# Kernel tuning notes

Measured on AMD Instinct MI355X. Metric: run time of the kernel, lower is better.

## Reference

```python
import jax, jax.numpy as jnp
import numpy as np

DIM = 256
HEADS = 8
DIM_HEAD = 32
WS = 8  # window_size
INNER = HEADS * DIM_HEAD
SCALE = DIM_HEAD ** -0.5


def _rel_indices():
    # (WS^2, WS^2, 2) relative position indices, shifted to be non-negative
    idx = np.array([[x, y] for x in range(WS) for y in range(WS)])
    rel = idx[None, :, :] - idx[:, None, :] + (WS - 1)
    return jnp.asarray(rel, dtype=jnp.int32)


def setup_inputs() -> dict:
    key = jax.random.key(0)
    k1, k2, k3, k4 = jax.random.split(key, 4)
    x = jax.random.normal(k1, (2, 4, 128, 128, DIM), dtype=jnp.float32)
    w_qkv = jax.random.normal(k2, (DIM, 3 * INNER), dtype=jnp.float32) * 0.02
    pos_emb = jax.random.normal(k3, (2 * WS - 1, 2 * WS - 1), dtype=jnp.float32)
    w_out = jax.random.normal(k4, (INNER, DIM), dtype=jnp.float32) * 0.02
    b_out = jnp.zeros((DIM,), dtype=jnp.float32)
    return {"x": x, "w_qkv": w_qkv, "pos_emb": pos_emb, "w_out": w_out, "b_out": b_out}


def reference(x, w_qkv, pos_emb, w_out, b_out):
    B, L, H, W, C = x.shape
    nh, nw = H // WS, W // WS
    qkv = x @ w_qkv  # (B,L,H,W,3*INNER)
    q, k, v = jnp.split(qkv, 3, axis=-1)

    def to_windows(t):
        # (B,L,H,W,INNER) -> (B,L,m,nh*nw,WS*WS,DIM_HEAD)
        t = t.reshape(B, L, nh, WS, nw, WS, HEADS, DIM_HEAD)
        t = t.transpose(0, 1, 6, 2, 4, 3, 5, 7)
        return t.reshape(B, L, HEADS, nh * nw, WS * WS, DIM_HEAD)

    q, k, v = to_windows(q), to_windows(k), to_windows(v)

    rel = _rel_indices()
    bias = pos_emb[rel[..., 0], rel[..., 1]]  # (WS^2, WS^2)

    dots = jnp.einsum('blmhic,blmhjc->blmhij', q, k) * SCALE + bias
    attn = jax.nn.softmax(dots, axis=-1)
    out = jnp.einsum('blmhij,blmhjc->blmhic', attn, v)

    # inverse window rearrange: (B,L,m,nh*nw,WS*WS,c) -> (B,L,H,W,INNER)
    out = out.reshape(B, L, HEADS, nh, nw, WS, WS, DIM_HEAD)
    out = out.transpose(0, 1, 3, 5, 4, 6, 2, 7).reshape(B, L, H, W, INNER)
    return out @ w_out + b_out
```

## Files before the change

### kernel.cpp

```cpp
#include <hip/hip_runtime.h>
#include <hip/hip_bf16.h>


typedef __attribute__((ext_vector_type(8))) short bf16x8;
typedef __attribute__((ext_vector_type(4))) float f32x4;

__device__ __forceinline__ f32x4 mfma16(bf16x8 a, bf16x8 b, f32x4 c) {
  return __builtin_amdgcn_mfma_f32_16x16x32_bf16(a, b, c, 0, 0, 0);
}

__device__ __forceinline__ unsigned short f2bf(float f) {
  __hip_bfloat16 h = __float2bfloat16(f);
  return *reinterpret_cast<unsigned short*>(&h);
}

__device__ __forceinline__ uint2 pack4(float a, float b, float c, float d) {
  union { unsigned short u[4]; uint2 v; } pk;
  pk.u[0] = f2bf(a); pk.u[1] = f2bf(b); pk.u[2] = f2bf(c); pk.u[3] = f2bf(d);
  return pk.v;
}

#define LOG2E 1.4426950408889634f
#define EXPSCALE (0.17677669529663687f * 1.4426950408889634f)

#define XSTR 264
#define VSTR 72
#define SSTR 72
#define OFF_A  0
#define OFF_B  18432
#define OFF_SC 35328
#define SMEM_ELTS 39936

__global__ void prep_kernel(const float* __restrict__ w_qkv,
                            const float* __restrict__ w_out,
                            const float* __restrict__ pos_emb,
                            unsigned short* __restrict__ wqkvT,
                            unsigned short* __restrict__ woutT,
                            float* __restrict__ bias64) {
  const int stride = gridDim.x * blockDim.x;
  const int tid = blockIdx.x * blockDim.x + threadIdx.x;
  for (int i = tid; i < 768 * 256; i += stride) {
    int n = i >> 8, k = i & 255;
    int off = ((((n >> 4) * 8 + (k >> 5)) * 4 + ((k >> 3) & 3)) * 16 + (n & 15)) * 8 + (k & 7);
    wqkvT[off] = f2bf(w_qkv[k * 768 + n]);
  }
  for (int i = tid; i < 256 * 256; i += stride) {
    int n = i >> 8, k = i & 255;
    int off = ((((n >> 4) * 8 + (k >> 5)) * 4 + ((k >> 3) & 3)) * 16 + (n & 15)) * 8 + (k & 7);
    woutT[off] = f2bf(w_out[k * 256 + n]);
  }
  for (int i = tid; i < 64 * 64; i += stride) {
    int a = i >> 6, b = i & 63;
    int d0 = (b >> 3) - (a >> 3) + 7;
    int d1 = (b & 7) - (a & 7) + 7;
    bias64[i] = pos_emb[d0 * 15 + d1] * LOG2E;
  }
}

template <bool SWAP>
__device__ __forceinline__ void qkv_gemm(f32x4 (&acc)[4][4],
                                         const unsigned short* __restrict__ x_lds,
                                         const unsigned short* __restrict__ wqkvT,
                                         int col0, int l15, int lq) {
  const f32x4 zero4 = {0.f, 0.f, 0.f, 0.f};
#pragma unroll
  for (int rt = 0; rt < 4; ++rt)
#pragma unroll
    for (int ct = 0; ct < 4; ++ct) acc[rt][ct] = zero4;

  bf16x8 aP[4], bP[4], aN[4], bN[4];
#pragma unroll
  for (int rt = 0; rt < 4; ++rt)
    aP[rt] = *(const bf16x8*)&x_lds[(rt * 16 + l15) * XSTR + lq * 8];
#pragma unroll
  for (int ct = 0; ct < 4; ++ct)
    bP[ct] = *(const bf16x8*)&wqkvT[(((col0 >> 4) + ct) * 32 + lq) * 128 + l15 * 8];
#pragma unroll
  for (int kk = 0; kk < 8; ++kk) {
    if (kk < 7) {
      const int ko = (kk + 1) * 32 + lq * 8;
#pragma unroll
      for (int rt = 0; rt < 4; ++rt)
        aN[rt] = *(const bf16x8*)&x_lds[(rt * 16 + l15) * XSTR + ko];
#pragma unroll
      for (int ct = 0; ct < 4; ++ct)
        bN[ct] = *(const bf16x8*)&wqkvT[((((col0 >> 4) + ct) * 8 + kk + 1) * 4 + lq) * 128 + l15 * 8];
    }
#pragma unroll
    for (int rt = 0; rt < 4; ++rt)
#pragma unroll
      for (int ct = 0; ct < 4; ++ct)
        acc[rt][ct] = SWAP ? mfma16(bP[ct], aP[rt], acc[rt][ct])
                           : mfma16(aP[rt], bP[ct], acc[rt][ct]);
#pragma unroll
    for (int rt = 0; rt < 4; ++rt) aP[rt] = aN[rt];
#pragma unroll
    for (int ct = 0; ct < 4; ++ct) bP[ct] = bN[ct];
  }
}

__global__ __launch_bounds__(256, 2)
void winattn_kernel(const float* __restrict__ x,
                    const unsigned short* __restrict__ wqkvT,
                    const unsigned short* __restrict__ woutT,
                    const float* __restrict__ bias64,
                    const float* __restrict__ b_out,
                    float* __restrict__ out) {
  __shared__ unsigned short smem[SMEM_ELTS];

  const int tid = threadIdx.x;
  const int lane = tid & 63;
  const int w = tid >> 6;
  const int l15 = lane & 15;
  const int lq = lane >> 4;

  const int bid = blockIdx.x;
  const int win = bid & 255;
  const int img = bid >> 8;
  const int wy = win >> 4, wx = win & 15;

  unsigned short* x_lds  = smem + OFF_A;
  unsigned short* vT_lds = smem + OFF_A;
  unsigned short* qk_lds = smem + OFF_B;
  unsigned short* sc = smem + OFF_SC + w * (16 * SSTR);

  const f32x4 zero4 = {0.f, 0.f, 0.f, 0.f};
  const size_t img_base = (size_t)img * 128 * 128 * 256;

  {
#pragma unroll
    for (int r = 0; r < 16; ++r) {
      int p = r * 4 + w;
      const float* src = x + img_base +
          (((size_t)(wy * 8 + (p >> 3)) * 128) + (wx * 8 + (p & 7))) * 256 + lane * 4;
      float4 v4 = *(const float4*)src;
      *(uint2*)&x_lds[p * XSTR + lane * 4] = pack4(v4.x, v4.y, v4.z, v4.w);
    }
  }
  __syncthreads();

  {
    f32x4 acc[4][4];
    qkv_gemm<true>(acc, x_lds, wqkvT, w * 64, l15, lq);
#pragma unroll
    for (int rt = 0; rt < 4; ++rt)
#pragma unroll
      for (int ct = 0; ct < 4; ++ct)
        *(uint2*)&qk_lds[(rt * 16 + l15) * XSTR + w * 64 + ct * 16 + lq * 4] =
            pack4(acc[rt][ct][0], acc[rt][ct][1], acc[rt][ct][2], acc[rt][ct][3]);
  }
  __syncthreads();

  bf16x8 qf[8];
#pragma unroll
  for (int h = 0; h < 8; ++h)
    qf[h] = *(const bf16x8*)&qk_lds[(w * 16 + l15) * XSTR + h * 32 + lq * 8];

  {
    f32x4 kacc[4][4];
    qkv_gemm<true>(kacc, x_lds, wqkvT, 256 + w * 64, l15, lq);
    __syncthreads();
#pragma unroll
    for (int rt = 0; rt < 4; ++rt)
#pragma unroll
      for (int ct = 0; ct < 4; ++ct)
        *(uint2*)&qk_lds[(rt * 16 + l15) * XSTR + w * 64 + ct * 16 + lq * 4] =
            pack4(kacc[rt][ct][0], kacc[rt][ct][1], kacc[rt][ct][2], kacc[rt][ct][3]);
  }

  {
    f32x4 vacc[4][4];
    qkv_gemm<false>(vacc, x_lds, wqkvT, 512 + w * 64, l15, lq);
    __syncthreads();
#pragma unroll
    for (int rt = 0; rt < 4; ++rt)
#pragma unroll
      for (int ct = 0; ct < 4; ++ct)
        *(uint2*)&vT_lds[(w * 64 + ct * 16 + l15) * VSTR + rt * 16 + lq * 4] =
            pack4(vacc[rt][ct][0], vacc[rt][ct][1], vacc[rt][ct][2], vacc[rt][ct][3]);
  }
  __syncthreads();

  f32x4 bias4[4];
#pragma unroll
  for (int rt = 0; rt < 4; ++rt)
    bias4[rt] = *(const f32x4*)&bias64[(w * 16 + l15) * 64 + rt * 16 + lq * 4];

  const short one_bf = (short)0x3F80;
  const bf16x8 ones = {one_bf, one_bf, one_bf, one_bf,
                       one_bf, one_bf, one_bf, one_bf};

  f32x4 ACC[16];
#pragma unroll
  for (int ct = 0; ct < 16; ++ct) ACC[ct] = zero4;

  f32x4 s_t[4];
#pragma unroll
  for (int rt = 0; rt < 4; ++rt) {
    const bf16x8 bk = *(const bf16x8*)&qk_lds[(rt * 16 + l15) * XSTR + lq * 8];
    f32x4 t = mfma16(bk, qf[0], zero4);
#pragma unroll
    for (int r = 0; r < 4; ++r)
      s_t[rt][r] = __builtin_amdgcn_exp2f(t[r] * EXPSCALE + bias4[rt][r]);
  }

#pragma unroll
  for (int h = 0; h < 8; ++h) {
#pragma unroll
    for (int rt = 0; rt < 4; ++rt)
      *(uint2*)&sc[l15 * SSTR + rt * 16 + lq * 4] =
          pack4(s_t[rt][0], s_t[rt][1], s_t[rt][2], s_t[rt][3]);

    f32x4 sn[4];
    if (h < 7) {
#pragma unroll
      for (int rt = 0; rt < 4; ++rt) {
        const bf16x8 bk = *(const bf16x8*)&qk_lds[(rt * 16 + l15) * XSTR + (h + 1) * 32 + lq * 8];
        f32x4 t = mfma16(bk, qf[h + 1], zero4);
#pragma unroll
        for (int r = 0; r < 4; ++r)
          sn[rt][r] = __builtin_amdgcn_exp2f(t[r] * EXPSCALE + bias4[rt][r]);
      }
    }

    const bf16x8 ap0 = *(const bf16x8*)&sc[l15 * SSTR + lq * 8];
    const bf16x8 ap1 = *(const bf16x8*)&sc[l15 * SSTR + 32 + lq * 8];
    bf16x8 bw[16];
#pragma unroll
    for (int ct = 0; ct < 16; ++ct)
      bw[ct] = *(const bf16x8*)&woutT[((ct * 8 + h) * 4 + lq) * 128 + l15 * 8];

    f32x4 o0 = zero4, o1 = zero4, osum = zero4;
    {
      const bf16x8 bv00 = *(const bf16x8*)&vT_lds[(h * 32 + l15) * VSTR + lq * 8];
      const bf16x8 bv01 = *(const bf16x8*)&vT_lds[(h * 32 + l15) * VSTR + 32 + lq * 8];
      const bf16x8 bv10 = *(const bf16x8*)&vT_lds[(h * 32 + 16 + l15) * VSTR + lq * 8];
      const bf16x8 bv11 = *(const bf16x8*)&vT_lds[(h * 32 + 16 + l15) * VSTR + 32 + lq * 8];
      o0 = mfma16(bv00, ap0, o0);  o0 = mfma16(bv01, ap1, o0);
      o1 = mfma16(bv10, ap0, o1);  o1 = mfma16(bv11, ap1, o1);
      osum = mfma16(ones, ap0, osum);
      osum = mfma16(ones, ap1, osum);
    }

    const float rinv = __builtin_amdgcn_rcpf(osum[0]);
    *(uint2*)&sc[l15 * SSTR + lq * 4] =
        pack4(o0[0] * rinv, o0[1] * rinv, o0[2] * rinv, o0[3] * rinv);
    *(uint2*)&sc[l15 * SSTR + 16 + lq * 4] =
        pack4(o1[0] * rinv, o1[1] * rinv, o1[2] * rinv, o1[3] * rinv);

    const bf16x8 ao = *(const bf16x8*)&sc[l15 * SSTR + lq * 8];
#pragma unroll
    for (int ct = 0; ct < 16; ++ct)
      ACC[ct] = mfma16(bw[ct], ao, ACC[ct]);

    if (h < 7) {
#pragma unroll
      for (int rt = 0; rt < 4; ++rt) s_t[rt] = sn[rt];
    }
  }

  {
    const int p = w * 16 + l15;
    float* orow = out + img_base +
        (((size_t)(wy * 8 + (p >> 3)) * 128) + (wx * 8 + (p & 7))) * 256;
#pragma unroll
    for (int ct = 0; ct < 16; ++ct) {
      const int n0 = ct * 16 + lq * 4;
      const f32x4 bo4 = *(const f32x4*)&b_out[n0];
      f32x4 st;
#pragma unroll
      for (int r = 0; r < 4; ++r) st[r] = ACC[ct][r] + bo4[r];
      *(f32x4*)(orow + n0) = st;
    }
  }
}

extern "C" void kernel_launch(void* const* d_in, const int* in_sizes, int n_in,
                              void* d_out, int out_size, void* d_ws, size_t ws_size,
                              hipStream_t stream) {
  const float* x       = (const float*)d_in[0];
  const float* w_qkv   = (const float*)d_in[1];
  const float* pos_emb = (const float*)d_in[2];
  const float* w_out   = (const float*)d_in[3];
  const float* b_out   = (const float*)d_in[4];
  float* out = (float*)d_out;

  unsigned short* wqkvT = (unsigned short*)d_ws;
  unsigned short* woutT = wqkvT + 768 * 256;
  float* bias64 = (float*)(woutT + 256 * 256);

  prep_kernel<<<96, 256, 0, stream>>>(w_qkv, w_out, pos_emb, wqkvT, woutT, bias64);
  winattn_kernel<<<2048, 256, 0, stream>>>(x, wqkvT, woutT, bias64, b_out, out);
}
```

Before: 132.4 us.

## Restructure window attention so each wave owns two heads, keeping Q/K/V in registers

Each wave now computes Q, K and V for its own two heads in 32-column chunks and moves them into MFMA fragment registers through a small per-wave LDS transpose buffer. Shared LDS staging of Q/K/V is gone, cutting LDS use enough to raise launch bounds to three blocks per CU. Softmax row sums now use cross-lane shuffles instead of an extra ones-MFMA. The output projection becomes a separate block-wide GEMM over head outputs staged in LDS, so the per-head woutT reloads disappear. In exchange the kernel carries more register pressure, drops the explicit software prefetch in the GEMM, and adds a synchronization before the final projection.

Measured after the change: 116.6 us (median of 2 runs). 1.14x faster.

```diff
diff --git a/kernel.cpp b/kernel.cpp
--- a/kernel.cpp
+++ b/kernel.cpp
@@ -23,13 +23,12 @@
 #define LOG2E 1.4426950408889634f
 #define EXPSCALE (0.17677669529663687f * 1.4426950408889634f)
 
-#define XSTR 264
-#define VSTR 72
-#define SSTR 72
-#define OFF_A  0
-#define OFF_B  18432
-#define OFF_SC 35328
-#define SMEM_ELTS 39936
+#define XO  264
+#define RTS 40
+#define PS  72
+#define RT_ELEMS 1280
+#define OFF_RT 16896
+#define SMEM_ELTS 22016
 
 __global__ void prep_kernel(const float* __restrict__ w_qkv,
                             const float* __restrict__ w_out,
@@ -58,48 +57,34 @@
 }
 
 template <bool SWAP>
-__device__ __forceinline__ void qkv_gemm(f32x4 (&acc)[4][4],
-                                         const unsigned short* __restrict__ x_lds,
-                                         const unsigned short* __restrict__ wqkvT,
-                                         int col0, int l15, int lq) {
+__device__ __forceinline__ void gemm32(f32x4 (&acc)[4][2],
+                                       const unsigned short* __restrict__ a_lds,
+                                       const unsigned short* __restrict__ wT,
+                                       int col0, int l15, int lq) {
   const f32x4 zero4 = {0.f, 0.f, 0.f, 0.f};
 #pragma unroll
   for (int rt = 0; rt < 4; ++rt)
 #pragma unroll
-    for (int ct = 0; ct < 4; ++ct) acc[rt][ct] = zero4;
-
-  bf16x8 aP[4], bP[4], aN[4], bN[4];
-#pragma unroll
-  for (int rt = 0; rt < 4; ++rt)
-    aP[rt] = *(const bf16x8*)&x_lds[(rt * 16 + l15) * XSTR + lq * 8];
-#pragma unroll
-  for (int ct = 0; ct < 4; ++ct)
-    bP[ct] = *(const bf16x8*)&wqkvT[(((col0 >> 4) + ct) * 32 + lq) * 128 + l15 * 8];
+    for (int ct = 0; ct < 2; ++ct) acc[rt][ct] = zero4;
 #pragma unroll
   for (int kk = 0; kk < 8; ++kk) {
-    if (kk < 7) {
-      const int ko = (kk + 1) * 32 + lq * 8;
-#pragma unroll
-      for (int rt = 0; rt < 4; ++rt)
-        aN[rt] = *(const bf16x8*)&x_lds[(rt * 16 + l15) * XSTR + ko];
-#pragma unroll
-      for (int ct = 0; ct < 4; ++ct)
-        bN[ct] = *(const bf16x8*)&wqkvT[((((col0 >> 4) + ct) * 8 + kk + 1) * 4 + lq) * 128 + l15 * 8];
-    }
+    bf16x8 a[4], b[2];
 #pragma unroll
     for (int rt = 0; rt < 4; ++rt)
-#pragma unroll
-      for (int ct = 0; ct < 4; ++ct)
-        acc[rt][ct] = SWAP ? mfma16(bP[ct], aP[rt], acc[rt][ct])
-                           : mfma16(aP[rt], bP[ct], acc[rt][ct]);
-#pragma unroll
-    for (int rt = 0; rt < 4; ++rt) aP[rt] = aN[rt];
-#pragma unroll
-    for (int ct = 0; ct < 4; ++ct) bP[ct] = bN[ct];
-  }
-}
-
-__global__ __launch_bounds__(256, 2)
+      a[rt] = *(const bf16x8*)&a_lds[(rt * 16 + l15) * XO + kk * 32 + lq * 8];
+#pragma unroll
+    for (int ct = 0; ct < 2; ++ct)
+      b[ct] = *(const bf16x8*)&wT[((((col0 >> 4) + ct) * 8 + kk) * 4 + lq) * 128 + l15 * 8];
+#pragma unroll
+    for (int rt = 0; rt < 4; ++rt)
+#pragma unroll
+      for (int ct = 0; ct < 2; ++ct)
+        acc[rt][ct] = SWAP ? mfma16(b[ct], a[rt], acc[rt][ct])
+                           : mfma16(a[rt], b[ct], acc[rt][ct]);
+  }
+}
+
+__global__ __launch_bounds__(256, 3)
 void winattn_kernel(const float* __restrict__ x,
                     const unsigned short* __restrict__ wqkvT,
                     const unsigned short* __restrict__ woutT,
@@ -119,10 +104,9 @@
   const int img = bid >> 8;
   const int wy = win >> 4, wx = win & 15;
 
-  unsigned short* x_lds  = smem + OFF_A;
-  unsigned short* vT_lds = smem + OFF_A;
-  unsigned short* qk_lds = smem + OFF_B;
-  unsigned short* sc = smem + OFF_SC + w * (16 * SSTR);
+  unsigned short* x_lds  = smem;
+  unsigned short* oh_lds = smem;
+  unsigned short* rt_buf = smem + OFF_RT + w * RT_ELEMS;
 
   const f32x4 zero4 = {0.f, 0.f, 0.f, 0.f};
   const size_t img_base = (size_t)img * 128 * 128 * 256;
@@ -134,143 +118,147 @@
       const float* src = x + img_base +
           (((size_t)(wy * 8 + (p >> 3)) * 128) + (wx * 8 + (p & 7))) * 256 + lane * 4;
       float4 v4 = *(const float4*)src;
-      *(uint2*)&x_lds[p * XSTR + lane * 4] = pack4(v4.x, v4.y, v4.z, v4.w);
+      *(uint2*)&x_lds[p * XO + lane * 4] = pack4(v4.x, v4.y, v4.z, v4.w);
     }
   }
   __syncthreads();
 
+  bf16x8 qf[4][2], kf[4][2], vf[2][2][2];
   {
-    f32x4 acc[4][4];
-    qkv_gemm<true>(acc, x_lds, wqkvT, w * 64, l15, lq);
+    f32x4 acc[4][2];
+#pragma unroll
+    for (int hh = 0; hh < 2; ++hh) {
+      gemm32<true>(acc, x_lds, wqkvT, w * 64 + hh * 32, l15, lq);
+#pragma unroll
+      for (int h2 = 0; h2 < 2; ++h2) {
+#pragma unroll
+        for (int rr = 0; rr < 2; ++rr)
+#pragma unroll
+          for (int ct = 0; ct < 2; ++ct)
+            *(uint2*)&rt_buf[(rr * 16 + l15) * RTS + ct * 16 + lq * 4] =
+                pack4(acc[h2 * 2 + rr][ct][0], acc[h2 * 2 + rr][ct][1],
+                      acc[h2 * 2 + rr][ct][2], acc[h2 * 2 + rr][ct][3]);
+#pragma unroll
+        for (int rr = 0; rr < 2; ++rr)
+          qf[h2 * 2 + rr][hh] = *(const bf16x8*)&rt_buf[(rr * 16 + l15) * RTS + lq * 8];
+      }
+    }
+#pragma unroll
+    for (int hh = 0; hh < 2; ++hh) {
+      gemm32<true>(acc, x_lds, wqkvT, 256 + w * 64 + hh * 32, l15, lq);
+#pragma unroll
+      for (int h2 = 0; h2 < 2; ++h2) {
+#pragma unroll
+        for (int rr = 0; rr < 2; ++rr)
+#pragma unroll
+          for (int ct = 0; ct < 2; ++ct)
+            *(uint2*)&rt_buf[(rr * 16 + l15) * RTS + ct * 16 + lq * 4] =
+                pack4(acc[h2 * 2 + rr][ct][0], acc[h2 * 2 + rr][ct][1],
+                      acc[h2 * 2 + rr][ct][2], acc[h2 * 2 + rr][ct][3]);
+#pragma unroll
+        for (int rr = 0; rr < 2; ++rr)
+          kf[h2 * 2 + rr][hh] = *(const bf16x8*)&rt_buf[(rr * 16 + l15) * RTS + lq * 8];
+      }
+    }
+#pragma unroll
+    for (int hh = 0; hh < 2; ++hh) {
+      gemm32<false>(acc, x_lds, wqkvT, 512 + w * 64 + hh * 32, l15, lq);
+#pragma unroll
+      for (int h2 = 0; h2 < 2; ++h2) {
+#pragma unroll
+        for (int rr = 0; rr < 2; ++rr)
+#pragma unroll
+          for (int ct = 0; ct < 2; ++ct)
+            *(uint2*)&rt_buf[(ct * 16 + l15) * RTS + rr * 16 + lq * 4] =
+                pack4(acc[h2 * 2 + rr][ct][0], acc[h2 * 2 + rr][ct][1],
+                      acc[h2 * 2 + rr][ct][2], acc[h2 * 2 + rr][ct][3]);
+#pragma unroll
+        for (int ft = 0; ft < 2; ++ft)
+          vf[ft][h2][hh] = *(const bf16x8*)&rt_buf[(ft * 16 + l15) * RTS + lq * 8];
+      }
+    }
+  }
+  __syncthreads();
+
+#pragma unroll
+  for (int it = 0; it < 4; ++it) {
+    f32x4 bias4[4];
+#pragma unroll
+    for (int jt = 0; jt < 4; ++jt)
+      bias4[jt] = *(const f32x4*)&bias64[(it * 16 + l15) * 64 + jt * 16 + lq * 4];
+#pragma unroll
+    for (int hh = 0; hh < 2; ++hh) {
+      f32x4 s[4];
+#pragma unroll
+      for (int jt = 0; jt < 4; ++jt)
+        s[jt] = mfma16(kf[jt][hh], qf[it][hh], zero4);
+      float rs = 0.f;
+#pragma unroll
+      for (int jt = 0; jt < 4; ++jt)
+#pragma unroll
+        for (int r = 0; r < 4; ++r) {
+          s[jt][r] = __builtin_amdgcn_exp2f(s[jt][r] * EXPSCALE + bias4[jt][r]);
+          rs += s[jt][r];
+        }
+      rs += __shfl_xor(rs, 16);
+      rs += __shfl_xor(rs, 32);
+      const float rinv = __builtin_amdgcn_rcpf(rs);
+
+#pragma unroll
+      for (int jt = 0; jt < 4; ++jt)
+        *(uint2*)&rt_buf[l15 * PS + jt * 16 + lq * 4] =
+            pack4(s[jt][0], s[jt][1], s[jt][2], s[jt][3]);
+      const bf16x8 ap0 = *(const bf16x8*)&rt_buf[l15 * PS + lq * 8];
+      const bf16x8 ap1 = *(const bf16x8*)&rt_buf[l15 * PS + 32 + lq * 8];
+
+      f32x4 o0 = mfma16(vf[0][0][hh], ap0, zero4);
+      o0 = mfma16(vf[0][1][hh], ap1, o0);
+      f32x4 o1 = mfma16(vf[1][0][hh], ap0, zero4);
+      o1 = mfma16(vf[1][1][hh], ap1, o1);
+
+      *(uint2*)&oh_lds[(it * 16 + l15) * XO + w * 64 + hh * 32 + lq * 4] =
+          pack4(o0[0] * rinv, o0[1] * rinv, o0[2] * rinv, o0[3] * rinv);
+      *(uint2*)&oh_lds[(it * 16 + l15) * XO + w * 64 + hh * 32 + 16 + lq * 4] =
+          pack4(o1[0] * rinv, o1[1] * rinv, o1[2] * rinv, o1[3] * rinv);
+    }
+  }
+  __syncthreads();
+
+  {
+    f32x4 ACC[4][4];
 #pragma unroll
     for (int rt = 0; rt < 4; ++rt)
 #pragma unroll
+      for (int ct = 0; ct < 4; ++ct) ACC[rt][ct] = zero4;
+#pragma unroll
+    for (int kk = 0; kk < 8; ++kk) {
+      bf16x8 a[4], b[4];
+#pragma unroll
+      for (int rt = 0; rt < 4; ++rt)
+        a[rt] = *(const bf16x8*)&oh_lds[(rt * 16 + l15) * XO + kk * 32 + lq * 8];
+#pragma unroll
       for (int ct = 0; ct < 4; ++ct)
-        *(uint2*)&qk_lds[(rt * 16 + l15) * XSTR + w * 64 + ct * 16 + lq * 4] =
-            pack4(acc[rt][ct][0], acc[rt][ct][1], acc[rt][ct][2], acc[rt][ct][3]);
-  }
-  __syncthreads();
-
-  bf16x8 qf[8];
-#pragma unroll
-  for (int h = 0; h < 8; ++h)
-    qf[h] = *(const bf16x8*)&qk_lds[(w * 16 + l15) * XSTR + h * 32 + lq * 8];
-
-  {
-    f32x4 kacc[4][4];
-    qkv_gemm<true>(kacc, x_lds, wqkvT, 256 + w * 64, l15, lq);
-    __syncthreads();
-#pragma unroll
-    for (int rt = 0; rt < 4; ++rt)
-#pragma unroll
-      for (int ct = 0; ct < 4; ++ct)
-        *(uint2*)&qk_lds[(rt * 16 + l15) * XSTR + w * 64 + ct * 16 + lq * 4] =
-            pack4(kacc[rt][ct][0], kacc[rt][ct][1], kacc[rt][ct][2], kacc[rt][ct][3]);
-  }
-
-  {
-    f32x4 vacc[4][4];
-    qkv_gemm<false>(vacc, x_lds, wqkvT, 512 + w * 64, l15, lq);
-    __syncthreads();
-#pragma unroll
-    for (int rt = 0; rt < 4; ++rt)
-#pragma unroll
-      for (int ct = 0; ct < 4; ++ct)
-        *(uint2*)&vT_lds[(w * 64 + ct * 16 + l15) * VSTR + rt * 16 + lq * 4] =
-            pack4(vacc[rt][ct][0], vacc[rt][ct][1], vacc[rt][ct][2], vacc[rt][ct][3]);
-  }
-  __syncthreads();
-
-  f32x4 bias4[4];
-#pragma unroll
-  for (int rt = 0; rt < 4; ++rt)
-    bias4[rt] = *(const f32x4*)&bias64[(w * 16 + l15) * 64 + rt * 16 + lq * 4];
-
-  const short one_bf = (short)0x3F80;
-  const bf16x8 ones = {one_bf, one_bf, one_bf, one_bf,
-                       one_bf, one_bf, one_bf, one_bf};
-
-  f32x4 ACC[16];
-#pragma unroll
-  for (int ct = 0; ct < 16; ++ct) ACC[ct] = zero4;
-
-  f32x4 s_t[4];
-#pragma unroll
-  for (int rt = 0; rt < 4; ++rt) {
-    const bf16x8 bk = *(const bf16x8*)&qk_lds[(rt * 16 + l15) * XSTR + lq * 8];
-    f32x4 t = mfma16(bk, qf[0], zero4);
-#pragma unroll
-    for (int r = 0; r < 4; ++r)
-      s_t[rt][r] = __builtin_amdgcn_exp2f(t[r] * EXPSCALE + bias4[rt][r]);
-  }
-
-#pragma unroll
-  for (int h = 0; h < 8; ++h) {
-#pragma unroll
-    for (int rt = 0; rt < 4; ++rt)
-      *(uint2*)&sc[l15 * SSTR + rt * 16 + lq * 4] =
-          pack4(s_t[rt][0], s_t[rt][1], s_t[rt][2], s_t[rt][3]);
-
-    f32x4 sn[4];
-    if (h < 7) {
-#pragma unroll
-      for (int rt = 0; rt < 4; ++rt) {
-        const bf16x8 bk = *(const bf16x8*)&qk_lds[(rt * 16 + l15) * XSTR + (h + 1) * 32 + lq * 8];
-        f32x4 t = mfma16(bk, qf[h + 1], zero4);
-#pragma unroll
-        for (int r = 0; r < 4; ++r)
-          sn[rt][r] = __builtin_amdgcn_exp2f(t[r] * EXPSCALE + bias4[rt][r]);
-      }
-    }
-
-    const bf16x8 ap0 = *(const bf16x8*)&sc[l15 * SSTR + lq * 8];
-    const bf16x8 ap1 = *(const bf16x8*)&sc[l15 * SSTR + 32 + lq * 8];
-    bf16x8 bw[16];
-#pragma unroll
-    for (int ct = 0; ct < 16; ++ct)
-      bw[ct] = *(const bf16x8*)&woutT[((ct * 8 + h) * 4 + lq) * 128 + l15 * 8];
-
-    f32x4 o0 = zero4, o1 = zero4, osum = zero4;
-    {
-      const bf16x8 bv00 = *(const bf16x8*)&vT_lds[(h * 32 + l15) * VSTR + lq * 8];
-      const bf16x8 bv01 = *(const bf16x8*)&vT_lds[(h * 32 + l15) * VSTR + 32 + lq * 8];
-      const bf16x8 bv10 = *(const bf16x8*)&vT_lds[(h * 32 + 16 + l15) * VSTR + lq * 8];
-      const bf16x8 bv11 = *(const bf16x8*)&vT_lds[(h * 32 + 16 + l15) * VSTR + 32 + lq * 8];
-      o0 = mfma16(bv00, ap0, o0);  o0 = mfma16(bv01, ap1, o0);
-      o1 = mfma16(bv10, ap0, o1);  o1 = mfma16(bv11, ap1, o1);
-      osum = mfma16(ones, ap0, osum);
-      osum = mfma16(ones, ap1, osum);
-    }
-
-    const float rinv = __builtin_amdgcn_rcpf(osum[0]);
-    *(uint2*)&sc[l15 * SSTR + lq * 4] =
-        pack4(o0[0] * rinv, o0[1] * rinv, o0[2] * rinv, o0[3] * rinv);
-    *(uint2*)&sc[l15 * SSTR + 16 + lq * 4] =
-        pack4(o1[0] * rinv, o1[1] * rinv, o1[2] * rinv, o1[3] * rinv);
-
-    const bf16x8 ao = *(const bf16x8*)&sc[l15 * SSTR + lq * 8];
-#pragma unroll
-    for (int ct = 0; ct < 16; ++ct)
-      ACC[ct] = mfma16(bw[ct], ao, ACC[ct]);
-
-    if (h < 7) {
-#pragma unroll
-      for (int rt = 0; rt < 4; ++rt) s_t[rt] = sn[rt];
-    }
-  }
-
-  {
-    const int p = w * 16 + l15;
-    float* orow = out + img_base +
-        (((size_t)(wy * 8 + (p >> 3)) * 128) + (wx * 8 + (p & 7))) * 256;
-#pragma unroll
-    for (int ct = 0; ct < 16; ++ct) {
-      const int n0 = ct * 16 + lq * 4;
-      const f32x4 bo4 = *(const f32x4*)&b_out[n0];
-      f32x4 st;
-#pragma unroll
-      for (int r = 0; r < 4; ++r) st[r] = ACC[ct][r] + bo4[r];
-      *(f32x4*)(orow + n0) = st;
+        b[ct] = *(const bf16x8*)&woutT[(((w * 4 + ct) * 8 + kk) * 4 + lq) * 128 + l15 * 8];
+#pragma unroll
+      for (int rt = 0; rt < 4; ++rt)
+#pragma unroll
+        for (int ct = 0; ct < 4; ++ct)
+          ACC[rt][ct] = mfma16(b[ct], a[rt], ACC[rt][ct]);
+    }
+#pragma unroll
+    for (int rt = 0; rt < 4; ++rt) {
+      const int p = rt * 16 + l15;
+      float* orow = out + img_base +
+          (((size_t)(wy * 8 + (p >> 3)) * 128) + (wx * 8 + (p & 7))) * 256;
+#pragma unroll
+      for (int ct = 0; ct < 4; ++ct) {
+        const int n0 = w * 64 + ct * 16 + lq * 4;
+        const f32x4 bo4 = *(const f32x4*)&b_out[n0];
+        f32x4 st;
+#pragma unroll
+        for (int r = 0; r < 4; ++r) st[r] = ACC[rt][ct][r] + bo4[r];
+        *(f32x4*)(orow + n0) = st;
+      }
     }
   }
 }
```
